# Kernel tuning notes

Hardware: AMD Instinct MI355X
Metric: run time of the kernel (lower is better)

Reference implementation:

```python
import jax, jax.numpy as jnp
import numpy as np

N, E = 50000, 1000000
H, Q, F, M = 128, 128, 64, 16  # hidden, equivariant, edge_feat, sh dims


def setup_inputs() -> dict:
    key = jax.random.key(0)
    ks = jax.random.split(key, 20)
    s = lambda fin: 1.0 / np.sqrt(fin)
    return {
        'h': jax.random.normal(ks[0], (N, H), jnp.float32),
        'h_eq': jax.random.normal(ks[1], (N, Q), jnp.float32),
        'edge_feat': jax.random.normal(ks[2], (E, F), jnp.float32),
        'sh': jax.random.normal(ks[3], (E, M), jnp.float32),
        'edge_i': jax.random.randint(ks[4], (E,), 0, N, jnp.int64),
        'edge_j': jax.random.randint(ks[5], (E,), 0, N, jnp.int64),
        # weights stored [in, out]; y = x @ W + b (equivalent to torch Linear)
        'W_in': jax.random.uniform(ks[6], (H, Q), jnp.float32, -s(H), s(H)),
        'b_in': jnp.zeros((Q,), jnp.float32),
        'W_gate': jax.random.uniform(ks[7], (H, Q), jnp.float32, -s(H), s(H)),
        'b_gate': jnp.zeros((Q,), jnp.float32),
        'W1': jax.random.uniform(ks[8], (H + F, H), jnp.float32, -s(H + F), s(H + F)),
        'b1': jnp.zeros((H,), jnp.float32),
        'W2': jax.random.uniform(ks[9], (H, H), jnp.float32, -s(H), s(H)),
        'b2': jnp.zeros((H,), jnp.float32),
        'W_up': jax.random.uniform(ks[10], (H, H), jnp.float32, -s(H), s(H)),
        'b_up': jnp.zeros((H,), jnp.float32),
        'W_tp': jax.random.uniform(ks[11], (M, Q), jnp.float32, -s(M), s(M)),
    }


def reference(h, h_eq, edge_feat, sh, edge_i, edge_j,
              W_in, b_in, W_gate, b_gate, W1, b1, W2, b2, W_up, b_up, W_tp):
    n_nodes = h.shape[0]
    # gather source node features: [E, H]
    h_j = h[edge_j]
    # scalar message MLP on concatenated [h_j, edge_feat]
    x = jnp.concatenate([h_j, edge_feat], axis=-1)
    scalar_msg = jax.nn.silu(x @ W1 + b1) @ W2 + b2  # [E, H]
    agg_scalar = jax.ops.segment_sum(scalar_msg, edge_i, num_segments=n_nodes)
    h_new = h + agg_scalar @ W_up + b_up
    # equivariant message: channel-wise tensor product with spherical harmonics
    eq_in = h_j @ W_in + b_in              # [E, Q]
    eq_msg = eq_in * (sh @ W_tp)           # [E, Q]
    agg_eq = jax.ops.segment_sum(eq_msg, edge_i, num_segments=n_nodes)
    gate = jax.nn.sigmoid(h_new @ W_gate + b_gate)  # gate uses UPDATED h
    h_eq_new = h_eq + agg_eq * gate
    return h_new, h_eq_new
```

## Files before the change

kernel.cpp:

```cpp
#include <hip/hip_runtime.h>
#include <hip/hip_bf16.h>


#define Hdim 128
#define Fdim 64
#define Mdim 16
#define TE   64
#define XLD  200
#define YLD  132
#define SLD  40

typedef __attribute__((ext_vector_type(8))) short short8;
typedef __attribute__((ext_vector_type(4))) short short4v;
typedef __attribute__((ext_vector_type(4))) float float4v;

__device__ __forceinline__ float b2f(short s) {
    union { unsigned u; float f; } c;
    c.u = ((unsigned)(unsigned short)s) << 16;
    return c.f;
}
__device__ __forceinline__ short f2b(float f) {
    union { __hip_bfloat16 h; short s; } c;
    c.h = __float2bfloat16(f);
    return c.s;
}
__device__ __forceinline__ float ldf(const void* p, long i, int isbf) {
    return isbf ? b2f(((const short*)p)[i]) : ((const float*)p)[i];
}
__device__ __forceinline__ int ldi(const void* p, long i, int is64) {
    return is64 ? (int)((const long long*)p)[i] : ((const int*)p)[i];
}

__global__ void ei_sniff_kernel(const unsigned* __restrict__ hw,
                                const unsigned* __restrict__ iw,
                                int* __restrict__ flags)
{
    __shared__ int cf[64], ci[64];
    const int t = threadIdx.x;
    int c1 = 0, c2 = 0;
#pragma unroll
    for (int k = 0; k < 4; ++k) {
        const unsigned w = hw[t + 64 * k];
        const unsigned e = (w >> 7) & 0xFFu;
        c1 += (e >= 100u && e <= 140u) ? 1 : 0;
        const unsigned wi = iw[2 * (t + 64 * k) + 1];
        c2 += (wi == 0u) ? 1 : 0;
    }
    cf[t] = c1; ci[t] = c2;
    __syncthreads();
    if (t == 0) {
        int s1 = 0, s2 = 0;
        for (int i = 0; i < 64; ++i) { s1 += cf[i]; s2 += ci[i]; }
        flags[0] = (s1 >= 192) ? 1 : 0;
        flags[1] = (s2 >= 200) ? 1 : 0;
    }
}


__global__ void ei_hist_kernel(const void* __restrict__ edge_i,
                               int* __restrict__ hist,
                               const int* __restrict__ flags, int E_)
{
    const int dti = flags[1];
    int i = blockIdx.x * blockDim.x + threadIdx.x;
    const int stride = gridDim.x * blockDim.x;
    for (; i < E_; i += stride) atomicAdd(&hist[ldi(edge_i, i, dti)], 1);
}

__global__ void ei_scan_kernel(int* __restrict__ hist,
                               int* __restrict__ rs, int N_, int E_)
{
    __shared__ int buf[1024];
    const int t = threadIdx.x;
    const int chunk = (N_ + 1023) >> 10;
    const int base = t * chunk;
    int s = 0;
    for (int i = 0; i < chunk; ++i) {
        const int idx = base + i;
        if (idx < N_) s += hist[idx];
    }
    buf[t] = s;
    __syncthreads();
    for (int d = 1; d < 1024; d <<= 1) {
        const int v = (t >= d) ? buf[t - d] : 0;
        __syncthreads();
        buf[t] += v;
        __syncthreads();
    }
    int run = buf[t] - s;
    for (int i = 0; i < chunk; ++i) {
        const int idx = base + i;
        if (idx >= N_) break;
        const int h = hist[idx];
        rs[idx] = run;
        hist[idx] = run;
        run += h;
    }
    if (t == 0) rs[N_] = E_;
}

__global__ void ei_scatter_kernel(const void* __restrict__ edge_i,
                                  int* __restrict__ cur,
                                  int* __restrict__ perm,
                                  const int* __restrict__ flags, int E_)
{
    const int dti = flags[1];
    int i = blockIdx.x * blockDim.x + threadIdx.x;
    const int stride = gridDim.x * blockDim.x;
    for (; i < E_; i += stride) {
        const int c = ldi(edge_i, i, dti);
        const int p = atomicAdd(&cur[c], 1);
        perm[p] = i;
    }
}

__global__ void ei_w2up_kernel(const void* __restrict__ W2,
                               const void* __restrict__ Wup,
                               const void* __restrict__ b2,
                               short* __restrict__ w2up,
                               float* __restrict__ bu2,
                               const int* __restrict__ flags)
{
    const int dtf = flags[0];
    const int o = threadIdx.x;
    const int i = blockIdx.x;
    float acc = 0.f;
    for (int m = 0; m < Hdim; ++m) {
        const float a = (i < Hdim) ? ldf(W2, (long)i * Hdim + m, dtf)
                                   : ldf(b2, m, dtf);
        acc += a * ldf(Wup, (long)m * Hdim + o, dtf);
    }
    if (i < Hdim) w2up[i * Hdim + o] = f2b(acc);
    else          bu2[o] = acc;
}

__global__ __launch_bounds__(256, 2)
void ei_edge_sorted(const void* __restrict__ hmat,
                    const void* __restrict__ efeat,
                    const void* __restrict__ shmat,
                    const void* __restrict__ edge_j,
                    const int*  __restrict__ perm,
                    const int*  __restrict__ edge_i_sorted_src,
                    const void* __restrict__ W1,
                    const void* __restrict__ b1,
                    const void* __restrict__ Win,
                    const void* __restrict__ bin,
                    const void* __restrict__ Wtp,
                    float* __restrict__ agg_y,
                    float* __restrict__ agg_q,
                    const int* __restrict__ flags,
                    int ntiles)
{
    __shared__ alignas(16) short Xs[TE][XLD];
    __shared__ alignas(16) short Ys[TE][YLD];
    __shared__ alignas(16) short Qs[TE][YLD];
    __shared__ alignas(16) short Ss[TE][SLD];
    __shared__ int ids[TE];

    const int dtf = flags[0];
    const int dti = flags[1];

    const int tid  = threadIdx.x;
    const int lane = tid & 63;
    const int wv   = tid >> 6;
    const int q    = lane >> 4;
    const int ln   = lane & 15;
    const int mch0 = wv * 32;

    for (int i = tid; i < TE * XLD; i += 256) ((short*)Xs)[i] = 0;
    for (int i = tid; i < TE * YLD; i += 256) ((short*)Ys)[i] = 0;
    for (int i = tid; i < TE * YLD; i += 256) ((short*)Qs)[i] = 0;
    for (int i = tid; i < TE * SLD; i += 256) ((short*)Ss)[i] = 0;
    __syncthreads();

    short8 w1f[6][2], wif[4][2], wtf[2];
    float4v b1v[2], biv[2];
#pragma unroll
    for (int mt = 0; mt < 2; ++mt) {
        const int m = mch0 + mt * 16 + ln;
#pragma unroll
        for (int kc = 0; kc < 6; ++kc) {
            short8 t;
            const int k0 = kc * 32 + q * 8;
#pragma unroll
            for (int j = 0; j < 8; ++j) t[j] = dtf ? ((const short*)W1)[(long)(k0 + j) * Hdim + m]
                                                   : f2b(((const float*)W1)[(long)(k0 + j) * Hdim + m]);
            w1f[kc][mt] = t;
        }
#pragma unroll
        for (int kc = 0; kc < 4; ++kc) {
            short8 u;
            const int k0 = kc * 32 + q * 8;
#pragma unroll
            for (int j = 0; j < 8; ++j) {
                const long idx = (long)(k0 + j) * Hdim + m;
                u[j] = dtf ? ((const short*)Win)[idx] : f2b(((const float*)Win)[idx]);
            }
            wif[kc][mt] = u;
        }
        {
            short8 t;
#pragma unroll
            for (int j = 0; j < 8; ++j) {
                const int k = q * 8 + j;
                t[j] = (k < Mdim) ? (dtf ? ((const short*)Wtp)[(long)k * Hdim + m]
                                         : f2b(((const float*)Wtp)[(long)k * Hdim + m]))
                                  : (short)0;
            }
            wtf[mt] = t;
        }
        const int cb = mch0 + mt * 16 + q * 4;
#pragma unroll
        for (int r = 0; r < 4; ++r) {
            b1v[mt][r] = ldf(b1, cb + r, dtf);
            biv[mt][r] = ldf(bin, cb + r, dtf);
        }
    }

    const int e_loc = tid >> 2;
    const int part  = tid & 3;

    for (int tile = blockIdx.x; tile < ntiles; tile += gridDim.x) {
        {
            const int es = tile * TE + e_loc;
            const int e  = perm[es];
            const int j  = ldi(edge_j, e, dti);
            if (dtf) {
                const uint4* hsrc = (const uint4*)((const short*)hmat + (long)j * Hdim);
                uint4* xd = (uint4*)&Xs[e_loc][part * 32];
#pragma unroll
                for (int i = 0; i < 4; ++i) xd[i] = hsrc[part * 4 + i];
                const uint4* fsrc = (const uint4*)((const short*)efeat + (long)e * Fdim);
                uint4* fd = (uint4*)&Xs[e_loc][Hdim + part * 16];
                fd[0] = fsrc[part * 2 + 0];
                fd[1] = fsrc[part * 2 + 1];
                if (part == 0) {
                    const uint4* ssrc = (const uint4*)((const short*)shmat + (long)e * Mdim);
                    ((uint4*)&Ss[e_loc][0])[0] = ssrc[0];
                    ((uint4*)&Ss[e_loc][0])[1] = ssrc[1];
                }
            } else {
                const float4v* hs = (const float4v*)((const float*)hmat + (long)j * Hdim + part * 32);
#pragma unroll
                for (int c = 0; c < 4; ++c) {
                    const float4v v0 = hs[2 * c], v1 = hs[2 * c + 1];
                    short8 t;
#pragma unroll
                    for (int r = 0; r < 4; ++r) { t[r] = f2b(v0[r]); t[4 + r] = f2b(v1[r]); }
                    *(short8*)&Xs[e_loc][part * 32 + c * 8] = t;
                }
                const float4v* fs = (const float4v*)((const float*)efeat + (long)e * Fdim + part * 16);
#pragma unroll
                for (int c = 0; c < 2; ++c) {
                    const float4v v0 = fs[2 * c], v1 = fs[2 * c + 1];
                    short8 t;
#pragma unroll
                    for (int r = 0; r < 4; ++r) { t[r] = f2b(v0[r]); t[4 + r] = f2b(v1[r]); }
                    *(short8*)&Xs[e_loc][Hdim + part * 16 + c * 8] = t;
                }
                if (part == 0) {
                    const float4v* ss = (const float4v*)((const float*)shmat + (long)e * Mdim);
#pragma unroll
                    for (int c = 0; c < 2; ++c) {
                        const float4v v0 = ss[2 * c], v1 = ss[2 * c + 1];
                        short8 t;
#pragma unroll
                        for (int r = 0; r < 4; ++r) { t[r] = f2b(v0[r]); t[4 + r] = f2b(v1[r]); }
                        *(short8*)&Ss[e_loc][c * 8] = t;
                    }
                }
            }
            if (tid < TE) {
                const int e2 = perm[tile * TE + tid];
                ids[tid] = ldi(edge_i_sorted_src, e2, dti);
            }
        }
        __syncthreads();

        float4v a1[2][4] = {};
#pragma unroll
        for (int kc = 0; kc < 6; ++kc) {
            short8 xb[4];
#pragma unroll
            for (int nt = 0; nt < 4; ++nt)
                xb[nt] = *(const short8*)&Xs[nt * 16 + ln][kc * 32 + q * 8];
#pragma unroll
            for (int nt = 0; nt < 4; ++nt)
#pragma unroll
                for (int mt = 0; mt < 2; ++mt)
                    a1[mt][nt] = __builtin_amdgcn_mfma_f32_16x16x32_bf16(
                        w1f[kc][mt], xb[nt], a1[mt][nt], 0, 0, 0);
        }
#pragma unroll
        for (int mt = 0; mt < 2; ++mt)
#pragma unroll
            for (int nt = 0; nt < 4; ++nt) {
                short4v p;
#pragma unroll
                for (int r = 0; r < 4; ++r) {
                    const float y = a1[mt][nt][r] + b1v[mt][r];
                    const float s = y / (1.f + __expf(-y));
                    p[r] = f2b(s);
                }
                *(short4v*)&Ys[nt * 16 + ln][mch0 + mt * 16 + q * 4] = p;
            }

        float4v a3[2][4] = {};
        float4v at[2][4] = {};
#pragma unroll
        for (int kc = 0; kc < 4; ++kc) {
            short8 xb[4];
#pragma unroll
            for (int nt = 0; nt < 4; ++nt)
                xb[nt] = *(const short8*)&Xs[nt * 16 + ln][kc * 32 + q * 8];
#pragma unroll
            for (int nt = 0; nt < 4; ++nt)
#pragma unroll
                for (int mt = 0; mt < 2; ++mt)
                    a3[mt][nt] = __builtin_amdgcn_mfma_f32_16x16x32_bf16(
                        wif[kc][mt], xb[nt], a3[mt][nt], 0, 0, 0);
        }
        {
            short8 sb[4];
#pragma unroll
            for (int nt = 0; nt < 4; ++nt)
                sb[nt] = *(const short8*)&Ss[nt * 16 + ln][q * 8];
#pragma unroll
            for (int nt = 0; nt < 4; ++nt)
#pragma unroll
                for (int mt = 0; mt < 2; ++mt)
                    at[mt][nt] = __builtin_amdgcn_mfma_f32_16x16x32_bf16(
                        wtf[mt], sb[nt], at[mt][nt], 0, 0, 0);
        }
#pragma unroll
        for (int mt = 0; mt < 2; ++mt)
#pragma unroll
            for (int nt = 0; nt < 4; ++nt) {
                short4v p;
#pragma unroll
                for (int r = 0; r < 4; ++r)
                    p[r] = f2b((a3[mt][nt][r] + biv[mt][r]) * at[mt][nt][r]);
                *(short4v*)&Qs[nt * 16 + ln][mch0 + mt * 16 + q * 4] = p;
            }
        __syncthreads();

        if (tid < 128) {
            const int qsel = tid >> 6;
            const int c2   = tid & 63;
            const short* srcb = qsel ? &Qs[0][0] : &Ys[0][0];
            float* agg = qsel ? agg_q : agg_y;
            float v0 = 0.f, v1 = 0.f;
            int run_start = 0;
            for (int e = 0; e < TE; ++e) {
                const unsigned w = *(const unsigned*)(srcb + e * YLD + 2 * c2);
                union { unsigned u; float f; } lo, hi;
                lo.u = w << 16;
                hi.u = w & 0xFFFF0000u;
                v0 += lo.f;
                v1 += hi.f;
                const int id = ids[e];
                const bool last = (e == TE - 1) || (ids[e + 1] != id);
                if (last) {
                    float* dst = agg + (long)id * Hdim + 2 * c2;
                    if (run_start == 0 || e == TE - 1) {
                        unsafeAtomicAdd(dst, v0);
                        unsafeAtomicAdd(dst + 1, v1);
                    } else {
                        dst[0] = v0;
                        dst[1] = v1;
                    }
                    v0 = 0.f; v1 = 0.f;
                    run_start = e + 1;
                }
            }
        }
        __syncthreads();
    }
}

__global__ __launch_bounds__(256, 2)
void ei_node_kernel(const void* __restrict__ hmat,
                    const void* __restrict__ heq,
                    const short* __restrict__ w2up,
                    const float* __restrict__ bu2,
                    const void* __restrict__ bup,
                    const void* __restrict__ Wg,
                    const void* __restrict__ bg,
                    const int*  __restrict__ rs,
                    const float* __restrict__ agg_y,
                    const float* __restrict__ agg_q,
                    void* __restrict__ outp,
                    const int* __restrict__ flags,
                    int N)
{
    __shared__ alignas(16) short Xa[TE][YLD];
    __shared__ alignas(16) short Yh[TE][YLD];
    __shared__ int degs[TE];

    const int dtf = flags[0];

    const int tid  = threadIdx.x;
    const int lane = tid & 63;
    const int wv   = tid >> 6;
    const int q    = lane >> 4;
    const int ln   = lane & 15;
    const int mch0 = wv * 32;

    short* outh_b = (short*)outp;
    short* outq_b = outh_b + (long)N * Hdim;
    float* outh_f = (float*)outp;
    float* outq_f = outh_f + (long)N * Hdim;

    short8 wcf[4][2], wgf[4][2];
    float4v bu2v[2], bupv[2], bgv[2];
#pragma unroll
    for (int mt = 0; mt < 2; ++mt) {
        const int m = mch0 + mt * 16 + ln;
#pragma unroll
        for (int kc = 0; kc < 4; ++kc) {
            short8 t, u;
            const int k0 = kc * 32 + q * 8;
#pragma unroll
            for (int j = 0; j < 8; ++j) {
                const long idx = (long)(k0 + j) * Hdim + m;
                t[j] = w2up[idx];
                u[j] = dtf ? ((const short*)Wg)[idx] : f2b(((const float*)Wg)[idx]);
            }
            wcf[kc][mt] = t;
            wgf[kc][mt] = u;
        }
        const int cb = mch0 + mt * 16 + q * 4;
#pragma unroll
        for (int r = 0; r < 4; ++r) {
            bu2v[mt][r] = bu2[cb + r];
            bupv[mt][r] = ldf(bup, cb + r, dtf);
            bgv[mt][r]  = ldf(bg, cb + r, dtf);
        }
    }

    const int e_loc = tid >> 2;
    const int part  = tid & 3;
    const int nb    = blockIdx.x * TE;

    {
        const int node = nb + e_loc;
        if (node < N) {
            const float4v* src = (const float4v*)(agg_y + (long)node * Hdim + part * 32);
#pragma unroll
            for (int c = 0; c < 4; ++c) {
                const float4v v0 = src[2 * c], v1 = src[2 * c + 1];
                short8 t;
#pragma unroll
                for (int r = 0; r < 4; ++r) { t[r] = f2b(v0[r]); t[4 + r] = f2b(v1[r]); }
                *(short8*)&Xa[e_loc][part * 32 + c * 8] = t;
            }
            if (part == 0) degs[e_loc] = rs[node + 1] - rs[node];
        } else {
            short8 z = {};
#pragma unroll
            for (int c = 0; c < 4; ++c)
                *(short8*)&Xa[e_loc][part * 32 + c * 8] = z;
            if (part == 0) degs[e_loc] = 0;
        }
    }
    __syncthreads();

    float4v au[2][4] = {};
#pragma unroll
    for (int kc = 0; kc < 4; ++kc) {
        short8 ab[4];
#pragma unroll
        for (int nt = 0; nt < 4; ++nt)
            ab[nt] = *(const short8*)&Xa[nt * 16 + ln][kc * 32 + q * 8];
#pragma unroll
        for (int nt = 0; nt < 4; ++nt)
#pragma unroll
            for (int mt = 0; mt < 2; ++mt)
                au[mt][nt] = __builtin_amdgcn_mfma_f32_16x16x32_bf16(
                    wcf[kc][mt], ab[nt], au[mt][nt], 0, 0, 0);
    }
#pragma unroll
    for (int mt = 0; mt < 2; ++mt)
#pragma unroll
        for (int nt = 0; nt < 4; ++nt) {
            const int nd = nb + nt * 16 + ln;
            const int ch = mch0 + mt * 16 + q * 4;
            short4v p;
            if (nd < N) {
                const float dg = (float)degs[nt * 16 + ln];
                float hv[4];
                if (dtf) {
                    const short4v x = *(const short4v*)((const short*)hmat + (long)nd * Hdim + ch);
#pragma unroll
                    for (int r = 0; r < 4; ++r) hv[r] = b2f(x[r]);
                } else {
                    const float4v x = *(const float4v*)((const float*)hmat + (long)nd * Hdim + ch);
#pragma unroll
                    for (int r = 0; r < 4; ++r) hv[r] = x[r];
                }
                float4v o;
#pragma unroll
                for (int r = 0; r < 4; ++r) {
                    o[r] = hv[r] + au[mt][nt][r] + dg * bu2v[mt][r] + bupv[mt][r];
                    p[r] = f2b(o[r]);
                }
                if (dtf) *(short4v*)(outh_b + (long)nd * Hdim + ch) = p;
                else     *(float4v*)(outh_f + (long)nd * Hdim + ch) = o;
            } else {
#pragma unroll
                for (int r = 0; r < 4; ++r) p[r] = 0;
            }
            *(short4v*)&Yh[nt * 16 + ln][ch] = p;
        }
    __syncthreads();

    float4v ag[2][4] = {};
#pragma unroll
    for (int kc = 0; kc < 4; ++kc) {
        short8 yb[4];
#pragma unroll
        for (int nt = 0; nt < 4; ++nt)
            yb[nt] = *(const short8*)&Yh[nt * 16 + ln][kc * 32 + q * 8];
#pragma unroll
        for (int nt = 0; nt < 4; ++nt)
#pragma unroll
            for (int mt = 0; mt < 2; ++mt)
                ag[mt][nt] = __builtin_amdgcn_mfma_f32_16x16x32_bf16(
                    wgf[kc][mt], yb[nt], ag[mt][nt], 0, 0, 0);
    }
#pragma unroll
    for (int mt = 0; mt < 2; ++mt)
#pragma unroll
        for (int nt = 0; nt < 4; ++nt) {
            const int nd = nb + nt * 16 + ln;
            if (nd >= N) continue;
            const int ch = mch0 + mt * 16 + q * 4;
            const float4v aq = *(const float4v*)(agg_q + (long)nd * Hdim + ch);
            float hev[4];
            if (dtf) {
                const short4v x = *(const short4v*)((const short*)heq + (long)nd * Hdim + ch);
#pragma unroll
                for (int r = 0; r < 4; ++r) hev[r] = b2f(x[r]);
            } else {
                const float4v x = *(const float4v*)((const float*)heq + (long)nd * Hdim + ch);
#pragma unroll
                for (int r = 0; r < 4; ++r) hev[r] = x[r];
            }
            short4v p;
            float4v o;
#pragma unroll
            for (int r = 0; r < 4; ++r) {
                const float g = 1.f / (1.f + __expf(-(ag[mt][nt][r] + bgv[mt][r])));
                o[r] = hev[r] + aq[r] * g;
                p[r] = f2b(o[r]);
            }
            if (dtf) *(short4v*)(outq_b + (long)nd * Hdim + ch) = p;
            else     *(float4v*)(outq_f + (long)nd * Hdim + ch) = o;
        }
}

extern "C" void kernel_launch(void* const* d_in, const int* in_sizes, int n_in,
                              void* d_out, int out_size, void* d_ws, size_t ws_size,
                              hipStream_t stream)
{
    (void)n_in; (void)out_size; (void)ws_size;
    const void* hmat  = d_in[0];
    const void* heq   = d_in[1];
    const void* efeat = d_in[2];
    const void* shm   = d_in[3];
    const void* ei    = d_in[4];
    const void* ej    = d_in[5];
    const void* Win   = d_in[6];
    const void* bin   = d_in[7];
    const void* Wg    = d_in[8];
    const void* bg    = d_in[9];
    const void* W1    = d_in[10];
    const void* b1    = d_in[11];
    const void* W2    = d_in[12];
    const void* b2    = d_in[13];
    const void* Wup   = d_in[14];
    const void* bup   = d_in[15];
    const void* Wtp   = d_in[16];

    const int N = in_sizes[0] / Hdim;
    const int E = in_sizes[2] / Fdim;

    auto al = [](size_t x) { return (x + 255) & ~(size_t)255; };
    size_t off = 8;
    off = al(off); const size_t rs_off   = off; off += (size_t)(N + 1) * 4;
    off = al(off); const size_t cur_off  = off; off += (size_t)N * 4;
    off = al(off); const size_t perm_off = off; off += (size_t)E * 4;
    off = al(off); const size_t aggy_off = off; off += (size_t)N * Hdim * 4;
    const size_t aggq_off = off;                     off += (size_t)N * Hdim * 4;
    off = al(off); const size_t w2_off   = off; off += (size_t)Hdim * Hdim * 2;
    off = al(off); const size_t bu2_off  = off; off += (size_t)Hdim * 4;

    char* w = (char*)d_ws;
    int*   flags = (int*)w;
    int*   rs    = (int*)(w + rs_off);
    int*   cur   = (int*)(w + cur_off);
    int*   perm  = (int*)(w + perm_off);
    float* aggy  = (float*)(w + aggy_off);
    float* aggq  = (float*)(w + aggq_off);
    short* w2up  = (short*)(w + w2_off);
    float* bu2   = (float*)(w + bu2_off);

    ei_sniff_kernel<<<1, 64, 0, stream>>>((const unsigned*)hmat, (const unsigned*)ei, flags);
    hipMemsetAsync(cur, 0, (size_t)N * 4, stream);
    hipMemsetAsync(aggy, 0, (size_t)2 * N * Hdim * 4, stream);
    ei_hist_kernel<<<256, 256, 0, stream>>>(ei, cur, flags, E);
    ei_scan_kernel<<<1, 1024, 0, stream>>>(cur, rs, N, E);
    ei_scatter_kernel<<<256, 256, 0, stream>>>(ei, cur, perm, flags, E);
    ei_w2up_kernel<<<Hdim + 1, Hdim, 0, stream>>>(W2, Wup, b2, w2up, bu2, flags);
    ei_edge_sorted<<<1024, 256, 0, stream>>>(hmat, efeat, shm, ej, perm, (const int*)ei,
                                             W1, b1, Win, bin, Wtp,
                                             aggy, aggq, flags, E / TE);
    ei_node_kernel<<<(N + TE - 1) / TE, 256, 0, stream>>>(
        hmat, heq, w2up, bu2, bup, Wg, bg, rs, aggy, aggq, d_out, flags, N);
}
```

Before: 1.194 ms.

## Software-prefetch next edge tile into registers and parallelize segmented reduction

The gather of the next tile's h_j, edge features and spherical harmonics is issued into registers while the current tile's MFMA work runs, then written to shared memory at the start of the next iteration. The segmented reduction now uses all 256 threads, splitting each tile into two halves and precomputing segment boundaries with a ballot. Shared-memory reads are batched and paired stores use float2. The grid is halved to 512 blocks so each block loops over more tiles, at the cost of higher register pressure and more atomics at half-tile boundaries.

```diff
diff --git a/kernel.cpp b/kernel.cpp
--- a/kernel.cpp
+++ b/kernel.cpp
@@ -29,6 +29,12 @@
 }
 __device__ __forceinline__ int ldi(const void* p, long i, int is64) {
     return is64 ? (int)((const long long*)p)[i] : ((const int*)p)[i];
+}
+__device__ __forceinline__ short8 pack8(const float4v a, const float4v b) {
+    short8 t;
+#pragma unroll
+    for (int r = 0; r < 4; ++r) { t[r] = f2b(a[r]); t[4 + r] = f2b(b[r]); }
+    return t;
 }
 
 __global__ void ei_sniff_kernel(const unsigned* __restrict__ hw,
@@ -220,62 +226,67 @@
     const int e_loc = tid >> 2;
     const int part  = tid & 3;
 
-    for (int tile = blockIdx.x; tile < ntiles; tile += gridDim.x) {
-        {
-            const int es = tile * TE + e_loc;
-            const int e  = perm[es];
-            const int j  = ldi(edge_j, e, dti);
-            if (dtf) {
-                const uint4* hsrc = (const uint4*)((const short*)hmat + (long)j * Hdim);
-                uint4* xd = (uint4*)&Xs[e_loc][part * 32];
-#pragma unroll
-                for (int i = 0; i < 4; ++i) xd[i] = hsrc[part * 4 + i];
-                const uint4* fsrc = (const uint4*)((const short*)efeat + (long)e * Fdim);
-                uint4* fd = (uint4*)&Xs[e_loc][Hdim + part * 16];
-                fd[0] = fsrc[part * 2 + 0];
-                fd[1] = fsrc[part * 2 + 1];
-                if (part == 0) {
-                    const uint4* ssrc = (const uint4*)((const short*)shmat + (long)e * Mdim);
-                    ((uint4*)&Ss[e_loc][0])[0] = ssrc[0];
-                    ((uint4*)&Ss[e_loc][0])[1] = ssrc[1];
-                }
-            } else {
-                const float4v* hs = (const float4v*)((const float*)hmat + (long)j * Hdim + part * 32);
-#pragma unroll
-                for (int c = 0; c < 4; ++c) {
-                    const float4v v0 = hs[2 * c], v1 = hs[2 * c + 1];
-                    short8 t;
-#pragma unroll
-                    for (int r = 0; r < 4; ++r) { t[r] = f2b(v0[r]); t[4 + r] = f2b(v1[r]); }
-                    *(short8*)&Xs[e_loc][part * 32 + c * 8] = t;
-                }
-                const float4v* fs = (const float4v*)((const float*)efeat + (long)e * Fdim + part * 16);
-#pragma unroll
-                for (int c = 0; c < 2; ++c) {
-                    const float4v v0 = fs[2 * c], v1 = fs[2 * c + 1];
-                    short8 t;
-#pragma unroll
-                    for (int r = 0; r < 4; ++r) { t[r] = f2b(v0[r]); t[4 + r] = f2b(v1[r]); }
-                    *(short8*)&Xs[e_loc][Hdim + part * 16 + c * 8] = t;
-                }
-                if (part == 0) {
-                    const float4v* ss = (const float4v*)((const float*)shmat + (long)e * Mdim);
-#pragma unroll
-                    for (int c = 0; c < 2; ++c) {
-                        const float4v v0 = ss[2 * c], v1 = ss[2 * c + 1];
-                        short8 t;
-#pragma unroll
-                        for (int r = 0; r < 4; ++r) { t[r] = f2b(v0[r]); t[4 + r] = f2b(v1[r]); }
-                        *(short8*)&Ss[e_loc][c * 8] = t;
-                    }
-                }
-            }
-            if (tid < TE) {
-                const int e2 = perm[tile * TE + tid];
-                ids[tid] = ldi(edge_i_sorted_src, e2, dti);
-            }
-        }
+    short8 xh[4];
+    short8 xf[2];
+    short8 xs2[2];
+    int nx_e = 0, nx_j = 0, nx_pid = 0;
+
+    auto prefA = [&](int t) {
+        const int base = t * TE;
+        nx_e = perm[base + e_loc];
+        nx_j = ldi(edge_j, nx_e, dti);
+        if (tid < TE) nx_pid = ldi(edge_i_sorted_src, perm[base + tid], dti);
+    };
+    auto prefB = [&]() {
+        if (dtf) {
+            const short8* hs = (const short8*)((const short*)hmat + (long)nx_j * Hdim);
+#pragma unroll
+            for (int c = 0; c < 4; ++c) xh[c] = hs[part * 4 + c];
+            const short8* fs = (const short8*)((const short*)efeat + (long)nx_e * Fdim);
+            xf[0] = fs[part * 2 + 0];
+            xf[1] = fs[part * 2 + 1];
+            if (part == 0) {
+                const short8* ss = (const short8*)((const short*)shmat + (long)nx_e * Mdim);
+                xs2[0] = ss[0];
+                xs2[1] = ss[1];
+            }
+        } else {
+            const float4v* hs = (const float4v*)((const float*)hmat + (long)nx_j * Hdim + part * 32);
+#pragma unroll
+            for (int c = 0; c < 4; ++c) xh[c] = pack8(hs[2 * c], hs[2 * c + 1]);
+            const float4v* fs = (const float4v*)((const float*)efeat + (long)nx_e * Fdim + part * 16);
+            xf[0] = pack8(fs[0], fs[1]);
+            xf[1] = pack8(fs[2], fs[3]);
+            if (part == 0) {
+                const float4v* ss = (const float4v*)((const float*)shmat + (long)nx_e * Mdim);
+                xs2[0] = pack8(ss[0], ss[1]);
+                xs2[1] = pack8(ss[2], ss[3]);
+            }
+        }
+    };
+
+    int tile = blockIdx.x;
+    if (tile < ntiles) { prefA(tile); prefB(); }
+
+    for (; tile < ntiles; tile += gridDim.x) {
+#pragma unroll
+        for (int c = 0; c < 4; ++c)
+            *(short8*)&Xs[e_loc][part * 32 + c * 8] = xh[c];
+        *(short8*)&Xs[e_loc][Hdim + part * 16]     = xf[0];
+        *(short8*)&Xs[e_loc][Hdim + part * 16 + 8] = xf[1];
+        if (part == 0) {
+            *(short8*)&Ss[e_loc][0] = xs2[0];
+            *(short8*)&Ss[e_loc][8] = xs2[1];
+        }
+        if (tid < TE) ids[tid] = nx_pid;
         __syncthreads();
+
+        const unsigned long long bmask =
+            __ballot((lane == 63) || (ids[lane + 1] != ids[lane]));
+
+        int nxt = tile + (int)gridDim.x;
+        if (nxt >= ntiles) nxt = tile;
+        prefA(nxt);
 
         float4v a1[2][4] = {};
 #pragma unroll
@@ -342,35 +353,47 @@
                     p[r] = f2b((a3[mt][nt][r] + biv[mt][r]) * at[mt][nt][r]);
                 *(short4v*)&Qs[nt * 16 + ln][mch0 + mt * 16 + q * 4] = p;
             }
+
+        prefB();
         __syncthreads();
 
-        if (tid < 128) {
-            const int qsel = tid >> 6;
+        {
+            const int half = tid >> 7;
+            const int qsel = (tid >> 6) & 1;
             const int c2   = tid & 63;
             const short* srcb = qsel ? &Qs[0][0] : &Ys[0][0];
             float* agg = qsel ? agg_q : agg_y;
+            const int e0 = half * 32;
             float v0 = 0.f, v1 = 0.f;
-            int run_start = 0;
-            for (int e = 0; e < TE; ++e) {
-                const unsigned w = *(const unsigned*)(srcb + e * YLD + 2 * c2);
-                union { unsigned u; float f; } lo, hi;
-                lo.u = w << 16;
-                hi.u = w & 0xFFFF0000u;
-                v0 += lo.f;
-                v1 += hi.f;
-                const int id = ids[e];
-                const bool last = (e == TE - 1) || (ids[e + 1] != id);
-                if (last) {
-                    float* dst = agg + (long)id * Hdim + 2 * c2;
-                    if (run_start == 0 || e == TE - 1) {
-                        unsafeAtomicAdd(dst, v0);
-                        unsafeAtomicAdd(dst + 1, v1);
-                    } else {
-                        dst[0] = v0;
-                        dst[1] = v1;
+            int run_start = e0;
+#pragma unroll
+            for (int eb = 0; eb < 4; ++eb) {
+                unsigned wb[8];
+#pragma unroll
+                for (int k = 0; k < 8; ++k)
+                    wb[k] = *(const unsigned*)(srcb + (e0 + eb * 8 + k) * YLD + 2 * c2);
+#pragma unroll
+                for (int k = 0; k < 8; ++k) {
+                    const int e = e0 + eb * 8 + k;
+                    union { unsigned u; float f; } lo, hi;
+                    lo.u = wb[k] << 16;
+                    hi.u = wb[k] & 0xFFFF0000u;
+                    v0 += lo.f;
+                    v1 += hi.f;
+                    const bool hend = (e == e0 + 31);
+                    if (hend || ((bmask >> e) & 1ull)) {
+                        const int id = ids[e];
+                        float* dst = agg + (long)id * Hdim + 2 * c2;
+                        if (hend || run_start == e0) {
+                            unsafeAtomicAdd(dst, v0);
+                            unsafeAtomicAdd(dst + 1, v1);
+                        } else {
+                            float2 st; st.x = v0; st.y = v1;
+                            *(float2*)dst = st;
+                        }
+                        v0 = 0.f; v1 = 0.f;
+                        run_start = e + 1;
                     }
-                    v0 = 0.f; v1 = 0.f;
-                    run_start = e + 1;
                 }
             }
         }
@@ -612,9 +635,9 @@
     ei_scan_kernel<<<1, 1024, 0, stream>>>(cur, rs, N, E);
     ei_scatter_kernel<<<256, 256, 0, stream>>>(ei, cur, perm, flags, E);
     ei_w2up_kernel<<<Hdim + 1, Hdim, 0, stream>>>(W2, Wup, b2, w2up, bu2, flags);
-    ei_edge_sorted<<<1024, 256, 0, stream>>>(hmat, efeat, shm, ej, perm, (const int*)ei,
-                                             W1, b1, Win, bin, Wtp,
-                                             aggy, aggq, flags, E / TE);
+    ei_edge_sorted<<<512, 256, 0, stream>>>(hmat, efeat, shm, ej, perm, (const int*)ei,
+                                            W1, b1, Win, bin, Wtp,
+                                            aggy, aggq, flags, E / TE);
     ei_node_kernel<<<(N + TE - 1) / TE, 256, 0, stream>>>(
         hmat, heq, w2up, bu2, bup, Wg, bg, rs, aggy, aggq, d_out, flags, N);
 }
```

New measurement: 1.063 ms. 1.12x faster.
